# Performance work log

Hardware: AMD Instinct MI355X
Metric: run time of the kernel (lower is better)

Reference implementation:

```python
import jax, jax.numpy as jnp
import numpy as np


def _pairwise_sqdist(x, y):
    # x: [B, Nx, D] (gts), y: [B, Ny, D] (preds)
    # P[b,i,j] = ||x[b,i]||^2 + ||y[b,j]||^2 - 2 <x[b,i], y[b,j]>
    rx = jnp.sum(x * x, axis=-1)  # [B, Nx]
    ry = jnp.sum(y * y, axis=-1)  # [B, Ny]
    zz = jnp.einsum('bid,bjd->bij', x, y)  # [B, Nx, Ny]
    return rx[:, :, None] + ry[:, None, :] - 2.0 * zz


def setup_inputs() -> dict:
    key = jax.random.key(0)
    k1, k2 = jax.random.split(key)
    B, N, D = 8, 8192, 3
    preds = jax.random.normal(k1, (B, N, D), dtype=jnp.float32)
    gts = jax.random.normal(k2, (B, N, D), dtype=jnp.float32)
    return {"preds": preds, "gts": gts}


def reference(preds, gts):
    # Original: P = batch_pairwise_dist(gts, preds) -> [B, N_gts, N_preds]
    P = _pairwise_sqdist(gts, preds)
    loss_1 = jnp.sum(jnp.min(P, axis=1))  # min over gts points, per pred point
    loss_2 = jnp.sum(jnp.min(P, axis=2))  # min over pred points, per gt point
    return loss_1 + loss_2
```

## Files before the change

kernel.cpp:

```cpp
#include <hip/hip_runtime.h>

#define NPTS   8192
#define NBATCH 8
#define BLKT   256
#define CHUNK  2048
#define NCHUNK (NPTS / CHUNK)

typedef __attribute__((ext_vector_type(8)))  short bf16x8;
typedef __attribute__((ext_vector_type(16))) float f32x16;

__device__ __forceinline__ void bsplit(float v, unsigned int& h, unsigned int& l) {
    unsigned int u = __float_as_uint(v);
    h = u >> 16;
    float rem = v - __uint_as_float(u & 0xFFFF0000u);
    l = __float_as_uint(rem) >> 16;
}


__global__ __launch_bounds__(BLKT, 2) void chamfer_r7(
    const float* __restrict__ preds,
    const float* __restrict__ gts,
    float* __restrict__ out)
{
    __shared__ uint4 lds4[(CHUNK * 16 + 256 * 16) / 8];
    __shared__ float wsum[4];
    unsigned short* lds = (unsigned short*)lds4;

    const int tid  = threadIdx.x;
    const int wave = tid >> 6;
    const int lane = tid & 63;
    const int n    = lane & 31;
    const int h    = lane >> 5;

    const int rchunk = blockIdx.x;
    const int batch  = blockIdx.y;
    const int dir    = blockIdx.z;

    const float* rows = ((dir == 0) ? gts   : preds) + (size_t)batch * NPTS * 3;
    const float* cols = ((dir == 0) ? preds : gts)   + (size_t)batch * NPTS * 3;
    const int ibase = rchunk * 256;
    const unsigned int ONE = 0x3F80u;

    const int B_LO = 0;
    const int B_HI = CHUNK * 8;
    const int A_LO = CHUNK * 16;
    const int A_HI = CHUNK * 16 + 2048;

    {
        int gi = ibase + tid;
        float x = rows[gi * 3 + 0], y = rows[gi * 3 + 1], z = rows[gi * 3 + 2];
        float g2 = x * x + y * y + z * z;
        unsigned int xh, xl, yh, yl, zh, zl, gh, gl;
        bsplit(x, xh, xl); bsplit(y, yh, yl); bsplit(z, zh, zl); bsplit(g2, gh, gl);
        ((uint4*)(lds + A_LO))[tid] = make_uint4(xh | (yh << 16), zh | (gh << 16),
                                                 ONE | (xh << 16), yh | (zh << 16));
        ((uint4*)(lds + A_HI))[tid] = make_uint4(gh | (ONE << 16), xl | (yl << 16),
                                                 zl | (gl << 16), 0u);
    }
    __syncthreads();

    bf16x8 afr[2];
    #pragma unroll
    for (int t = 0; t < 2; ++t) {
        int row = wave * 64 + t * 32 + n;
        afr[t] = *(const bf16x8*)&lds[(h ? A_HI : A_LO) + row * 8];
    }
    f32x16 rmin[2];
    #pragma unroll
    for (int t = 0; t < 2; ++t)
        #pragma unroll
        for (int e = 0; e < 16; ++e) rmin[t][e] = 3.4e38f;
    __syncthreads();

    const f32x16 zeroC = (f32x16)(0.f);

    for (int ch = 0; ch < NCHUNK; ++ch) {
        #pragma unroll
        for (int j = 0; j < CHUNK / BLKT; ++j) {
            int c  = j * BLKT + tid;
            int gc = ch * CHUNK + c;
            float x = cols[gc * 3 + 0], y = cols[gc * 3 + 1], z = cols[gc * 3 + 2];
            float p2 = x * x + y * y + z * z;
            unsigned int cxh, cxl, cyh, cyl, czh, czl, ph, pl;
            bsplit(-2.f * x, cxh, cxl); bsplit(-2.f * y, cyh, cyl);
            bsplit(-2.f * z, czh, czl); bsplit(p2, ph, pl);
            ((uint4*)(lds + B_LO))[c] = make_uint4(cxh | (cyh << 16), czh | (ONE << 16),
                                                   ph | (cxl << 16), cyl | (czl << 16));
            ((uint4*)(lds + B_HI))[c] = make_uint4(pl << 16, cxh | (cyh << 16),
                                                   czh | (ONE << 16), ph);
        }
        __syncthreads();

        const unsigned short* bp = &lds[(h ? B_HI : B_LO) + n * 8];

        #pragma unroll 8
        for (int jt2 = 0; jt2 < CHUNK / 64; ++jt2) {
            bf16x8 b0 = *(const bf16x8*)(bp + (jt2 * 2 + 0) * 256);
            bf16x8 b1 = *(const bf16x8*)(bp + (jt2 * 2 + 1) * 256);
            f32x16 c0a = __builtin_amdgcn_mfma_f32_32x32x16_bf16(afr[0], b0, zeroC, 0, 0, 0);
            f32x16 c0b = __builtin_amdgcn_mfma_f32_32x32x16_bf16(afr[0], b1, zeroC, 0, 0, 0);
            f32x16 c1a = __builtin_amdgcn_mfma_f32_32x32x16_bf16(afr[1], b0, zeroC, 0, 0, 0);
            f32x16 c1b = __builtin_amdgcn_mfma_f32_32x32x16_bf16(afr[1], b1, zeroC, 0, 0, 0);
            #pragma unroll
            for (int e = 0; e < 16; ++e) {
                rmin[0][e] = fminf(fminf(c0a[e], c0b[e]), rmin[0][e]);
                rmin[1][e] = fminf(fminf(c1a[e], c1b[e]), rmin[1][e]);
            }
        }
        __syncthreads();
    }

    float s = 0.f;
    #pragma unroll
    for (int t = 0; t < 2; ++t) {
        #pragma unroll
        for (int e = 0; e < 16; ++e) {
            float v = rmin[t][e];
            v = fminf(v, __shfl_xor(v, 1, 64));
            v = fminf(v, __shfl_xor(v, 2, 64));
            v = fminf(v, __shfl_xor(v, 4, 64));
            v = fminf(v, __shfl_xor(v, 8, 64));
            v = fminf(v, __shfl_xor(v, 16, 64));
            if (n == 0) s += v;
        }
    }
    #pragma unroll
    for (int off = 32; off > 0; off >>= 1)
        s += __shfl_down(s, off, 64);
    if (lane == 0) wsum[wave] = s;
    __syncthreads();
    if (tid == 0)
        atomicAdd(out, wsum[0] + wsum[1] + wsum[2] + wsum[3]);
}

extern "C" void kernel_launch(void* const* d_in, const int* in_sizes, int n_in,
                              void* d_out, int out_size, void* d_ws, size_t ws_size,
                              hipStream_t stream) {
    const float* preds = (const float*)d_in[0];
    const float* gts   = (const float*)d_in[1];
    float* out = (float*)d_out;

    dim3 grid(NPTS / 256, NBATCH, 2);
    chamfer_r7<<<grid, dim3(BLKT), 0, stream>>>(preds, gts, out);
}
```

Before: 93.26 us.

## Fuse both chamfer directions into one pass with atomic column minima

Each distance tile is now computed once rather than once per direction. Row minima stay in registers. Column minima are reduced with a tree of fminf, combined through LDS atomicMin on the float bit pattern, then flushed to a global workspace with atomicMin. A small second kernel sums the column minima, and the workspace is reset by a memset before the main kernel. This halves the MFMA work but adds extra VALU reductions, LDS and global atomics, and two extra launches. Comparing floats as unsigned integers is only correct for non-negative values, and the bf16-split distances can come out slightly negative.

```diff
diff --git a/kernel.cpp b/kernel.cpp
--- a/kernel.cpp
+++ b/kernel.cpp
@@ -3,6 +3,7 @@
 #define NPTS   8192
 #define NBATCH 8
 #define BLKT   256
+#define RPB    128
 #define CHUNK  2048
 #define NCHUNK (NPTS / CHUNK)
 
@@ -16,6 +17,142 @@
     l = __float_as_uint(rem) >> 16;
 }
 
+__device__ __forceinline__ float tree16(const f32x16 c) {
+    float a = fminf(fminf(c[0],  c[1]),  c[2]);
+    float b = fminf(fminf(c[3],  c[4]),  c[5]);
+    float d = fminf(fminf(c[6],  c[7]),  c[8]);
+    float e = fminf(fminf(c[9],  c[10]), c[11]);
+    float f = fminf(fminf(c[12], c[13]), c[14]);
+    a = fminf(fminf(a, b), d);
+    e = fminf(fminf(e, f), c[15]);
+    return fminf(a, e);
+}
+
+__global__ __launch_bounds__(BLKT, 2) void chamfer_fused(
+    const float* __restrict__ preds,
+    const float* __restrict__ gts,
+    unsigned int* __restrict__ gcol,
+    float* __restrict__ out)
+{
+    __shared__ uint4 lds4[(CHUNK * 16 + RPB * 16) / 8];
+    __shared__ unsigned int cmin[CHUNK];
+    __shared__ float wsum[4];
+    unsigned short* lds = (unsigned short*)lds4;
+
+    const int tid  = threadIdx.x;
+    const int wave = tid >> 6;
+    const int lane = tid & 63;
+    const int n    = lane & 31;
+    const int h    = lane >> 5;
+
+    const int rchunk = blockIdx.x;
+    const int batch  = blockIdx.y;
+
+    const float* rows = gts   + (size_t)batch * NPTS * 3;
+    const float* cols = preds + (size_t)batch * NPTS * 3;
+    const int ibase = rchunk * RPB;
+    const unsigned int ONE = 0x3F80u;
+
+    const int B_LO = 0;
+    const int B_HI = CHUNK * 8;
+    const int A_LO = CHUNK * 16;
+    const int A_HI = CHUNK * 16 + RPB * 8;
+
+    if (tid < RPB) {
+        int gi = ibase + tid;
+        float x = rows[gi * 3 + 0], y = rows[gi * 3 + 1], z = rows[gi * 3 + 2];
+        float g2 = x * x + y * y + z * z;
+        unsigned int xh, xl, yh, yl, zh, zl, gh, gl;
+        bsplit(x, xh, xl); bsplit(y, yh, yl); bsplit(z, zh, zl); bsplit(g2, gh, gl);
+        ((uint4*)(lds + A_LO))[tid] = make_uint4(xh | (yh << 16), zh | (gh << 16),
+                                                 ONE | (xh << 16), yh | (zh << 16));
+        ((uint4*)(lds + A_HI))[tid] = make_uint4(gh | (ONE << 16), xl | (yl << 16),
+                                                 zl | (gl << 16), 0u);
+    }
+    for (int i = tid; i < CHUNK; i += BLKT) cmin[i] = 0x7F7FFFFFu;
+    __syncthreads();
+
+    bf16x8 afr = *(const bf16x8*)&lds[(h ? A_HI : A_LO) + (wave * 32 + n) * 8];
+    f32x16 rmin;
+    #pragma unroll
+    for (int e = 0; e < 16; ++e) rmin[e] = 3.4e38f;
+
+    const f32x16 zeroC = (f32x16)(0.f);
+
+    for (int ch = 0; ch < NCHUNK; ++ch) {
+        #pragma unroll
+        for (int j = 0; j < CHUNK / BLKT; ++j) {
+            int c  = j * BLKT + tid;
+            int gc = ch * CHUNK + c;
+            float x = cols[gc * 3 + 0], y = cols[gc * 3 + 1], z = cols[gc * 3 + 2];
+            float p2 = x * x + y * y + z * z;
+            unsigned int cxh, cxl, cyh, cyl, czh, czl, ph, pl;
+            bsplit(-2.f * x, cxh, cxl); bsplit(-2.f * y, cyh, cyl);
+            bsplit(-2.f * z, czh, czl); bsplit(p2, ph, pl);
+            ((uint4*)(lds + B_LO))[c] = make_uint4(cxh | (cyh << 16), czh | (ONE << 16),
+                                                   ph | (cxl << 16), cyl | (czl << 16));
+            ((uint4*)(lds + B_HI))[c] = make_uint4(pl << 16, cxh | (cyh << 16),
+                                                   czh | (ONE << 16), ph);
+        }
+        __syncthreads();
+
+        const unsigned short* bp = &lds[(h ? B_HI : B_LO) + n * 8];
+
+        #pragma unroll 8
+        for (int jt2 = 0; jt2 < CHUNK / 64; ++jt2) {
+            bf16x8 b0 = *(const bf16x8*)(bp + (jt2 * 2 + 0) * 256);
+            bf16x8 b1 = *(const bf16x8*)(bp + (jt2 * 2 + 1) * 256);
+            f32x16 ca = __builtin_amdgcn_mfma_f32_32x32x16_bf16(afr, b0, zeroC, 0, 0, 0);
+            f32x16 cb = __builtin_amdgcn_mfma_f32_32x32x16_bf16(afr, b1, zeroC, 0, 0, 0);
+            #pragma unroll
+            for (int e = 0; e < 16; ++e)
+                rmin[e] = fminf(fminf(ca[e], cb[e]), rmin[e]);
+            float va = tree16(ca), vb = tree16(cb);
+            atomicMin(&cmin[jt2 * 64 + n],      __float_as_uint(va));
+            atomicMin(&cmin[jt2 * 64 + 32 + n], __float_as_uint(vb));
+        }
+        __syncthreads();
+
+        unsigned int* g2 = gcol + (size_t)batch * NPTS + ch * CHUNK;
+        for (int i = tid; i < CHUNK; i += BLKT) {
+            atomicMin(&g2[i], cmin[i]);
+            cmin[i] = 0x7F7FFFFFu;
+        }
+    }
+
+    float s = 0.f;
+    #pragma unroll
+    for (int e = 0; e < 16; ++e) {
+        float v = rmin[e];
+        v = fminf(v, __shfl_xor(v, 1, 64));
+        v = fminf(v, __shfl_xor(v, 2, 64));
+        v = fminf(v, __shfl_xor(v, 4, 64));
+        v = fminf(v, __shfl_xor(v, 8, 64));
+        v = fminf(v, __shfl_xor(v, 16, 64));
+        if (n == 0) s += v;
+    }
+    #pragma unroll
+    for (int off = 32; off > 0; off >>= 1)
+        s += __shfl_down(s, off, 64);
+    if (lane == 0) wsum[wave] = s;
+    __syncthreads();
+    if (tid == 0)
+        atomicAdd(out, wsum[0] + wsum[1] + wsum[2] + wsum[3]);
+}
+
+__global__ void chamfer_colsum(const unsigned int* __restrict__ gcol,
+                               float* __restrict__ out)
+{
+    int i0 = blockIdx.x * blockDim.x + threadIdx.x;
+    float s = 0.f;
+    for (int i = i0; i < NBATCH * NPTS; i += gridDim.x * blockDim.x)
+        s += __uint_as_float(gcol[i]);
+    #pragma unroll
+    for (int off = 32; off > 0; off >>= 1)
+        s += __shfl_down(s, off, 64);
+    if ((threadIdx.x & 63) == 0)
+        atomicAdd(out, s);
+}
 
 __global__ __launch_bounds__(BLKT, 2) void chamfer_r7(
     const float* __restrict__ preds,
@@ -140,6 +277,15 @@
     const float* gts   = (const float*)d_in[1];
     float* out = (float*)d_out;
 
-    dim3 grid(NPTS / 256, NBATCH, 2);
-    chamfer_r7<<<grid, dim3(BLKT), 0, stream>>>(preds, gts, out);
-}
+    const size_t need = (size_t)NBATCH * NPTS * sizeof(unsigned int);
+    if (ws_size >= need) {
+        hipMemsetAsync(d_ws, 0xFF, need, stream);
+        chamfer_fused<<<dim3(NPTS / RPB, NBATCH), dim3(BLKT), 0, stream>>>(
+            preds, gts, (unsigned int*)d_ws, out);
+        chamfer_colsum<<<dim3(128), dim3(256), 0, stream>>>(
+            (const unsigned int*)d_ws, out);
+    } else {
+        dim3 grid(NPTS / 256, NBATCH, 2);
+        chamfer_r7<<<grid, dim3(BLKT), 0, stream>>>(preds, gts, out);
+    }
+}
```

Result: slower. 106.4 us (+14.1%).
